# Performance work log

Hardware: AMD Instinct MI355X
Metric: run time of the kernel (lower is better)

The kernel has to match this reference:

```python
import jax, jax.numpy as jnp
import numpy as np

B, L, S, D, H = 32, 256, 64, 128, 4
DH = D // H
EPS = 1e-5


def _uniform(k, shape, scale):
    return jax.random.uniform(k, shape, jnp.float32, -scale, scale)


def setup_inputs() -> dict:
    key = jax.random.key(0)
    ks = jax.random.split(key, 12)
    sc = 1.0 / np.sqrt(D)
    return {
        "h_wq": jax.random.normal(ks[0], (B, L, D), jnp.float32),
        "h_all": jax.random.normal(ks[1], (B, L, S, D), jnp.float32),
        "station_id": jax.random.randint(ks[2], (B,), 0, S),
        "adj": jax.random.randint(ks[3], (S, S), 0, 2).astype(jnp.float32),
        "in_proj_w": _uniform(ks[4], (3 * D, D), sc),
        "in_proj_b": _uniform(ks[5], (3 * D,), sc),
        "out_w": _uniform(ks[6], (D, D), sc),
        "out_b": _uniform(ks[7], (D,), sc),
        "gate_w": _uniform(ks[8], (D, 2 * D), 1.0 / np.sqrt(2 * D)),
        "gate_b": _uniform(ks[9], (D,), 1.0 / np.sqrt(2 * D)),
        "ln_g": jnp.ones((D,), jnp.float32),
        "ln_b": jnp.zeros((D,), jnp.float32),
        "alpha": jnp.asarray(0.1, jnp.float32),
    }


def _allowed_mask(adj, station_id):
    # allowed[b, s] == True  <=> station s may attend as key for sample b
    sid = station_id.astype(jnp.int32)
    allowed = adj[sid] > 0.0                                  # [B, S]
    self_oh = jax.nn.one_hot(sid, adj.shape[0], dtype=bool)   # [B, S]
    allowed = allowed & ~self_oh                              # exclude self
    # fallback-to-all for rows with no neighbor (still excluding self)
    no_nb = ~jnp.any(allowed, axis=1, keepdims=True)
    allowed = jnp.where(no_nb, ~self_oh, allowed)
    # final safety: if STILL empty (S==1 edge case), allow self
    no_nb2 = ~jnp.any(allowed, axis=1, keepdims=True)
    allowed = allowed | (no_nb2 & self_oh)
    return allowed


def _forward(h_wq, h_all, station_id, adj, in_proj_w, in_proj_b,
             out_w, out_b, gate_w, gate_b, ln_g, ln_b, alpha):
    b, l, d = h_wq.shape
    s = h_all.shape[2]
    qw, kw, vw = jnp.split(in_proj_w, 3, axis=0)
    qb, kb, vb = jnp.split(in_proj_b, 3, axis=0)

    q = (h_wq @ qw.T + qb).reshape(b, l, H, DH)        # [B,L,H,DH]
    k = (h_all @ kw.T + kb).reshape(b, l, s, H, DH)    # [B,L,S,H,DH]
    v = (h_all @ vw.T + vb).reshape(b, l, s, H, DH)

    scores = jnp.einsum('blhd,blshd->blhs', q, k) / np.sqrt(DH)  # [B,L,H,S]
    allowed = _allowed_mask(adj, station_id)                     # [B,S]
    scores = jnp.where(allowed[:, None, None, :], scores, -jnp.inf)
    w = jax.nn.softmax(scores, axis=-1)

    ctx = jnp.einsum('blhs,blshd->blhd', w, v).reshape(b, l, d)
    ctx = ctx @ out_w.T + out_b                                  # out_proj

    g = jax.nn.sigmoid(jnp.concatenate([h_wq, ctx], axis=-1) @ gate_w.T + gate_b)
    y = h_wq + alpha * (g * ctx)                                 # dropout = eval mode

    mu = jnp.mean(y, axis=-1, keepdims=True)
    var = jnp.mean(jnp.square(y - mu), axis=-1, keepdims=True)
    return (y - mu) * jax.lax.rsqrt(var + EPS) * ln_g + ln_b


def reference(h_wq, h_all, station_id, adj, in_proj_w, in_proj_b,
              out_w, out_b, gate_w, gate_b, ln_g, ln_b, alpha):
    return _forward(h_wq, h_all, station_id, adj, in_proj_w, in_proj_b,
                    out_w, out_b, gate_w, gate_b, ln_g, ln_b, alpha)
```

## Files before the change

### kernel.cpp

```cpp
#include <hip/hip_runtime.h>
#include <math.h>

#define B_   32
#define L_   256
#define S_   64
#define D_   128
#define NTOK (B_*L_)
#define TPB  8

__global__ __launch_bounds__(256) void fused_kernel(
        const float* __restrict__ h_wq,  const float* __restrict__ h_all,
        const int* __restrict__ station_id, const float* __restrict__ adj,
        const float* __restrict__ in_proj_w, const float* __restrict__ in_proj_b,
        const float* __restrict__ out_w,  const float* __restrict__ out_b,
        const float* __restrict__ gate_w, const float* __restrict__ gate_b,
        const float* __restrict__ ln_g,   const float* __restrict__ ln_b,
        const float* __restrict__ alpha,  float* __restrict__ out) {
    __shared__ float X[TPB*132];
    __shared__ float QK[TPB*528];
    __shared__ float A[TPB*528];
    __shared__ float cb[TPB][4];
    __shared__ int   lst[64];
    __shared__ int   cnt_s;

    const int t0  = blockIdx.x * TPB;
    const int b   = t0 >> 8;
    const int tid = threadIdx.x;
    const int wv  = tid >> 6, lane = tid & 63;
    const int d   = tid & 127, pr = tid >> 7;
    const int tb  = 4*pr;
    const float scale = 0.17677669529663687f;

    if (tid < 64) {
        int sid = station_id[b];
        int s = tid;
        bool av = (adj[sid*S_ + s] > 0.0f) && (s != sid);
        unsigned long long m = __ballot(av);
        if (m == 0ull) { av = (s != sid); m = __ballot(av); }
        if (m == 0ull) { av = (s == sid); m = __ballot(av); }
        int idx = __popcll(m & ((1ull << s) - 1ull));
        if (av) lst[idx] = s;
        if (s == 0) cnt_s = __popcll(m);
    }
    {
        int tok = tid >> 5, d4 = tid & 31;
        *(float4*)&X[tok*132 + d4*4] =
            *(const float4*)(h_wq + (size_t)(t0 + tok)*128 + d4*4);
    }
    __syncthreads();

    {
        const float4* wrow = (const float4*)(in_proj_w + (size_t)d*128);
        const float qb = in_proj_b[d];
        float a0 = qb, a1 = qb, a2 = qb, a3 = qb;
        const float *x0 = &X[(tb+0)*132], *x1 = &X[(tb+1)*132];
        const float *x2 = &X[(tb+2)*132], *x3 = &X[(tb+3)*132];
        #pragma unroll 8
        for (int j4 = 0; j4 < 32; ++j4) {
            float4 w  = wrow[j4];
            float4 u0 = *(const float4*)(x0 + j4*4);
            float4 u1 = *(const float4*)(x1 + j4*4);
            float4 u2 = *(const float4*)(x2 + j4*4);
            float4 u3 = *(const float4*)(x3 + j4*4);
            a0 += w.x*u0.x + w.y*u0.y + w.z*u0.z + w.w*u0.w;
            a1 += w.x*u1.x + w.y*u1.y + w.z*u1.z + w.w*u1.w;
            a2 += w.x*u2.x + w.y*u2.y + w.z*u2.z + w.w*u2.w;
            a3 += w.x*u3.x + w.y*u3.y + w.z*u3.z + w.w*u3.w;
        }
        A[(tb+0)*132 + d] = a0;  A[(tb+1)*132 + d] = a1;
        A[(tb+2)*132 + d] = a2;  A[(tb+3)*132 + d] = a3;
    }
    __syncthreads();

    {
        #pragma unroll
        for (int h = 0; h < 4; ++h) {
            float a0 = 0.f, a1 = 0.f, a2 = 0.f, a3 = 0.f;
            const float* wcol = in_proj_w + (size_t)(128 + h*32)*128 + d;
            #pragma unroll 8
            for (int j = 0; j < 32; ++j) {
                float w = wcol[(size_t)j*128];
                a0 += w * A[(tb+0)*132 + h*32 + j];
                a1 += w * A[(tb+1)*132 + h*32 + j];
                a2 += w * A[(tb+2)*132 + h*32 + j];
                a3 += w * A[(tb+3)*132 + h*32 + j];
            }
            QK[(tb+0)*528 + h*132 + d] = a0 * scale;
            QK[(tb+1)*528 + h*132 + d] = a1 * scale;
            QK[(tb+2)*528 + h*132 + d] = a2 * scale;
            QK[(tb+3)*528 + h*132 + d] = a3 * scale;
        }
    }
    if (tid < 32) {
        int tok = tid >> 2, h = tid & 3;
        float s = 0.f;
        for (int j = 0; j < 32; ++j)
            s += A[tok*132 + h*32 + j] * in_proj_b[128 + h*32 + j];
        cb[tok][h] = s * scale;
    }
    __syncthreads();

    {
        const int cnt = cnt_s;
        #pragma unroll
        for (int k = 0; k < 2; ++k) {
            const int tl = 2*wv + k;
            const int ridx = lst[lane < cnt ? lane : 0];
            const float* base = h_all + (size_t)(t0 + tl)*(S_*D_);
            const float* rp = base + (size_t)ridx*D_;
            const float* qkb = &QK[tl*528];

            float s0 = cb[tl][0], s1 = cb[tl][1], s2 = cb[tl][2], s3 = cb[tl][3];
            #pragma unroll 8
            for (int j4 = 0; j4 < 32; ++j4) {
                float4 x  = *(const float4*)(rp + j4*4);
                float4 w0 = *(const float4*)(qkb + 0*132 + j4*4);
                float4 w1 = *(const float4*)(qkb + 1*132 + j4*4);
                float4 w2 = *(const float4*)(qkb + 2*132 + j4*4);
                float4 w3 = *(const float4*)(qkb + 3*132 + j4*4);
                s0 += w0.x*x.x + w0.y*x.y + w0.z*x.z + w0.w*x.w;
                s1 += w1.x*x.x + w1.y*x.y + w1.z*x.z + w1.w*x.w;
                s2 += w2.x*x.x + w2.y*x.y + w2.z*x.z + w2.w*x.w;
                s3 += w3.x*x.x + w3.y*x.y + w3.z*x.z + w3.w*x.w;
            }
            const bool act = (lane < cnt);
            if (!act) { s0 = s1 = s2 = s3 = -INFINITY; }

            float m0 = s0, m1 = s1, m2 = s2, m3 = s3;
            #pragma unroll
            for (int o = 32; o >= 1; o >>= 1) {
                m0 = fmaxf(m0, __shfl_xor(m0, o));
                m1 = fmaxf(m1, __shfl_xor(m1, o));
                m2 = fmaxf(m2, __shfl_xor(m2, o));
                m3 = fmaxf(m3, __shfl_xor(m3, o));
            }
            float p0 = act ? __expf(s0 - m0) : 0.f;
            float p1 = act ? __expf(s1 - m1) : 0.f;
            float p2 = act ? __expf(s2 - m2) : 0.f;
            float p3 = act ? __expf(s3 - m3) : 0.f;
            float q0 = p0, q1 = p1, q2 = p2, q3 = p3;
            #pragma unroll
            for (int o = 32; o >= 1; o >>= 1) {
                q0 += __shfl_xor(q0, o);
                q1 += __shfl_xor(q1, o);
                q2 += __shfl_xor(q2, o);
                q3 += __shfl_xor(q3, o);
            }
            float4 wv4;
            wv4.x = p0 / q0; wv4.y = p1 / q1; wv4.z = p2 / q2; wv4.w = p3 / q3;
            *(float4*)&QK[tl*528 + lane*4] = wv4;

            float2 u0 = {0,0}, u1 = {0,0}, u2 = {0,0}, u3 = {0,0};
            for (int i = 0; i < cnt; ++i) {
                float2 x = *(const float2*)(base + (size_t)lst[i]*D_ + 2*lane);
                float4 w = *(const float4*)&QK[tl*528 + i*4];
                u0.x += w.x*x.x; u0.y += w.x*x.y;
                u1.x += w.y*x.x; u1.y += w.y*x.y;
                u2.x += w.z*x.x; u2.y += w.z*x.y;
                u3.x += w.w*x.x; u3.y += w.w*x.y;
            }
            *(float2*)&A[tl*528 + 0*132 + 2*lane] = u0;
            *(float2*)&A[tl*528 + 1*132 + 2*lane] = u1;
            *(float2*)&A[tl*528 + 2*132 + 2*lane] = u2;
            *(float2*)&A[tl*528 + 3*132 + 2*lane] = u3;
        }
    }
    __syncthreads();

    {
        const int h = d >> 5;
        const float4* vwrow = (const float4*)(in_proj_w + (size_t)(256 + d)*128);
        const float vb = in_proj_b[256 + d];
        float a0 = vb, a1 = vb, a2 = vb, a3 = vb;
        const float *u0 = &A[(tb+0)*528 + h*132], *u1 = &A[(tb+1)*528 + h*132];
        const float *u2 = &A[(tb+2)*528 + h*132], *u3 = &A[(tb+3)*528 + h*132];
        #pragma unroll 8
        for (int j4 = 0; j4 < 32; ++j4) {
            float4 w  = vwrow[j4];
            float4 v0 = *(const float4*)(u0 + j4*4);
            float4 v1 = *(const float4*)(u1 + j4*4);
            float4 v2 = *(const float4*)(u2 + j4*4);
            float4 v3 = *(const float4*)(u3 + j4*4);
            a0 += w.x*v0.x + w.y*v0.y + w.z*v0.z + w.w*v0.w;
            a1 += w.x*v1.x + w.y*v1.y + w.z*v1.z + w.w*v1.w;
            a2 += w.x*v2.x + w.y*v2.y + w.z*v2.z + w.w*v2.w;
            a3 += w.x*v3.x + w.y*v3.y + w.z*v3.z + w.w*v3.w;
        }
        QK[(tb+0)*132 + d] = a0;  QK[(tb+1)*132 + d] = a1;
        QK[(tb+2)*132 + d] = a2;  QK[(tb+3)*132 + d] = a3;
    }
    __syncthreads();

    {
        const float4* wrow = (const float4*)(out_w + (size_t)d*128);
        const float ob = out_b[d];
        float a0 = ob, a1 = ob, a2 = ob, a3 = ob;
        const float *c0 = &QK[(tb+0)*132], *c1 = &QK[(tb+1)*132];
        const float *c2 = &QK[(tb+2)*132], *c3 = &QK[(tb+3)*132];
        #pragma unroll 8
        for (int j4 = 0; j4 < 32; ++j4) {
            float4 w  = wrow[j4];
            float4 v0 = *(const float4*)(c0 + j4*4);
            float4 v1 = *(const float4*)(c1 + j4*4);
            float4 v2 = *(const float4*)(c2 + j4*4);
            float4 v3 = *(const float4*)(c3 + j4*4);
            a0 += w.x*v0.x + w.y*v0.y + w.z*v0.z + w.w*v0.w;
            a1 += w.x*v1.x + w.y*v1.y + w.z*v1.z + w.w*v1.w;
            a2 += w.x*v2.x + w.y*v2.y + w.z*v2.z + w.w*v2.w;
            a3 += w.x*v3.x + w.y*v3.y + w.z*v3.z + w.w*v3.w;
        }
        __syncthreads();
        A[(tb+0)*132 + d] = a0;  A[(tb+1)*132 + d] = a1;
        A[(tb+2)*132 + d] = a2;  A[(tb+3)*132 + d] = a3;
    }
    __syncthreads();

    {
        const float4* wrow = (const float4*)(gate_w + (size_t)d*256);
        const float gb = gate_b[d];
        float g0 = gb, g1 = gb, g2 = gb, g3 = gb;
        const float *x0 = &X[(tb+0)*132], *x1 = &X[(tb+1)*132];
        const float *x2 = &X[(tb+2)*132], *x3 = &X[(tb+3)*132];
        const float *o0 = &A[(tb+0)*132], *o1 = &A[(tb+1)*132];
        const float *o2 = &A[(tb+2)*132], *o3 = &A[(tb+3)*132];
        #pragma unroll 4
        for (int j4 = 0; j4 < 32; ++j4) {
            float4 wx = wrow[j4];
            float4 wo = wrow[32 + j4];
            float4 a, o;
            a = *(const float4*)(x0 + j4*4); o = *(const float4*)(o0 + j4*4);
            g0 += wx.x*a.x + wx.y*a.y + wx.z*a.z + wx.w*a.w
                + wo.x*o.x + wo.y*o.y + wo.z*o.z + wo.w*o.w;
            a = *(const float4*)(x1 + j4*4); o = *(const float4*)(o1 + j4*4);
            g1 += wx.x*a.x + wx.y*a.y + wx.z*a.z + wx.w*a.w
                + wo.x*o.x + wo.y*o.y + wo.z*o.z + wo.w*o.w;
            a = *(const float4*)(x2 + j4*4); o = *(const float4*)(o2 + j4*4);
            g2 += wx.x*a.x + wx.y*a.y + wx.z*a.z + wx.w*a.w
                + wo.x*o.x + wo.y*o.y + wo.z*o.z + wo.w*o.w;
            a = *(const float4*)(x3 + j4*4); o = *(const float4*)(o3 + j4*4);
            g3 += wx.x*a.x + wx.y*a.y + wx.z*a.z + wx.w*a.w
                + wo.x*o.x + wo.y*o.y + wo.z*o.z + wo.w*o.w;
        }
        const float al = alpha[0];
        float s0 = 1.0f/(1.0f + __expf(-g0)), s1 = 1.0f/(1.0f + __expf(-g1));
        float s2 = 1.0f/(1.0f + __expf(-g2)), s3 = 1.0f/(1.0f + __expf(-g3));
        QK[1056 + (tb+0)*132 + d] = x0[d] + al*s0*o0[d];
        QK[1056 + (tb+1)*132 + d] = x1[d] + al*s1*o1[d];
        QK[1056 + (tb+2)*132 + d] = x2[d] + al*s2*o2[d];
        QK[1056 + (tb+3)*132 + d] = x3[d] + al*s3*o3[d];
    }
    __syncthreads();

    {
        #pragma unroll
        for (int k = 0; k < 2; ++k) {
            const int tl = 2*wv + k;
            float y0 = QK[1056 + tl*132 + lane];
            float y1 = QK[1056 + tl*132 + 64 + lane];
            float s = y0 + y1;
            #pragma unroll
            for (int o = 32; o >= 1; o >>= 1) s += __shfl_xor(s, o);
            float mu = s * (1.0f/128.0f);
            float d0 = y0 - mu, d1 = y1 - mu;
            float v = d0*d0 + d1*d1;
            #pragma unroll
            for (int o = 32; o >= 1; o >>= 1) v += __shfl_xor(v, o);
            float rs = rsqrtf(v*(1.0f/128.0f) + 1e-5f);
            out[(size_t)(t0 + tl)*128 + lane]      = d0*rs*ln_g[lane]    + ln_b[lane];
            out[(size_t)(t0 + tl)*128 + 64 + lane] = d1*rs*ln_g[64+lane] + ln_b[64+lane];
        }
    }
}

extern "C" void kernel_launch(void* const* d_in, const int* in_sizes, int n_in,
                              void* d_out, int out_size, void* d_ws, size_t ws_size,
                              hipStream_t stream) {
    const float* h_wq       = (const float*)d_in[0];
    const float* h_all      = (const float*)d_in[1];
    const int*   station_id = (const int*)  d_in[2];
    const float* adj        = (const float*)d_in[3];
    const float* in_proj_w  = (const float*)d_in[4];
    const float* in_proj_b  = (const float*)d_in[5];
    const float* out_w      = (const float*)d_in[6];
    const float* out_b      = (const float*)d_in[7];
    const float* gate_w     = (const float*)d_in[8];
    const float* gate_b     = (const float*)d_in[9];
    const float* ln_g       = (const float*)d_in[10];
    const float* ln_b       = (const float*)d_in[11];
    const float* alpha      = (const float*)d_in[12];
    float* out = (float*)d_out;

    fused_kernel<<<NTOK/TPB, 256, 0, stream>>>(
        h_wq, h_all, station_id, adj, in_proj_w, in_proj_b,
        out_w, out_b, gate_w, gate_b, ln_g, ln_b, alpha, out);
}
```

Baseline: 440.4 us.

## Compute attention scores with coalesced row loads and 16-lane shuffle reductions

Restructures the score computation so each 16-lane group handles one head and the wave loops over active neighbor rows, loading each h_all row contiguously instead of having each lane stream its own row. Partial dot products are reduced with width-16 xor shuffles and written to shared memory, then reloaded per lane for the softmax. This targets the uncoalesced per-lane row reads of h_all. In exchange it adds a serial loop over neighbors with shuffle reductions and an extra __syncthreads to protect the QK buffer reuse.

New measurement: 457.6 us. +3.9%, slower.

```diff
diff --git a/kernel.cpp b/kernel.cpp
--- a/kernel.cpp
+++ b/kernel.cpp
@@ -102,31 +102,32 @@
 
     {
         const int cnt = cnt_s;
+        const int g  = lane >> 4, lg = lane & 15;
         #pragma unroll
         for (int k = 0; k < 2; ++k) {
             const int tl = 2*wv + k;
-            const int ridx = lst[lane < cnt ? lane : 0];
             const float* base = h_all + (size_t)(t0 + tl)*(S_*D_);
-            const float* rp = base + (size_t)ridx*D_;
-            const float* qkb = &QK[tl*528];
-
-            float s0 = cb[tl][0], s1 = cb[tl][1], s2 = cb[tl][2], s3 = cb[tl][3];
-            #pragma unroll 8
-            for (int j4 = 0; j4 < 32; ++j4) {
-                float4 x  = *(const float4*)(rp + j4*4);
-                float4 w0 = *(const float4*)(qkb + 0*132 + j4*4);
-                float4 w1 = *(const float4*)(qkb + 1*132 + j4*4);
-                float4 w2 = *(const float4*)(qkb + 2*132 + j4*4);
-                float4 w3 = *(const float4*)(qkb + 3*132 + j4*4);
-                s0 += w0.x*x.x + w0.y*x.y + w0.z*x.z + w0.w*x.w;
-                s1 += w1.x*x.x + w1.y*x.y + w1.z*x.z + w1.w*x.w;
-                s2 += w2.x*x.x + w2.y*x.y + w2.z*x.z + w2.w*x.w;
-                s3 += w3.x*x.x + w3.y*x.y + w3.z*x.z + w3.w*x.w;
-            }
-            const bool act = (lane < cnt);
-            if (!act) { s0 = s1 = s2 = s3 = -INFINITY; }
-
-            float m0 = s0, m1 = s1, m2 = s2, m3 = s3;
+            const float4 qa  = *(const float4*)&QK[tl*528 + g*132 + 4*lg];
+            const float4 qb2 = *(const float4*)&QK[tl*528 + g*132 + 64 + 4*lg];
+            const float cbg = cb[tl][g];
+
+            for (int i = 0; i < cnt; ++i) {
+                const float* rp = base + (size_t)lst[i]*D_;
+                float4 xa = *(const float4*)(rp + 4*lg);
+                float4 xb = *(const float4*)(rp + 64 + 4*lg);
+                float p = qa.x*xa.x + qa.y*xa.y + qa.z*xa.z + qa.w*xa.w
+                        + qb2.x*xb.x + qb2.y*xb.y + qb2.z*xb.z + qb2.w*xb.w;
+                p += __shfl_xor(p, 8, 16);
+                p += __shfl_xor(p, 4, 16);
+                p += __shfl_xor(p, 2, 16);
+                p += __shfl_xor(p, 1, 16);
+                if (lg == 0) A[tl*528 + i*4 + g] = p + cbg;
+            }
+
+            float4 s4;
+            if (lane < cnt) s4 = *(const float4*)&A[tl*528 + lane*4];
+            else { s4.x = -INFINITY; s4.y = -INFINITY; s4.z = -INFINITY; s4.w = -INFINITY; }
+            float m0 = s4.x, m1 = s4.y, m2 = s4.z, m3 = s4.w;
             #pragma unroll
             for (int o = 32; o >= 1; o >>= 1) {
                 m0 = fmaxf(m0, __shfl_xor(m0, o));
@@ -134,10 +135,11 @@
                 m2 = fmaxf(m2, __shfl_xor(m2, o));
                 m3 = fmaxf(m3, __shfl_xor(m3, o));
             }
-            float p0 = act ? __expf(s0 - m0) : 0.f;
-            float p1 = act ? __expf(s1 - m1) : 0.f;
-            float p2 = act ? __expf(s2 - m2) : 0.f;
-            float p3 = act ? __expf(s3 - m3) : 0.f;
+            const bool act = (lane < cnt);
+            float p0 = act ? __expf(s4.x - m0) : 0.f;
+            float p1 = act ? __expf(s4.y - m1) : 0.f;
+            float p2 = act ? __expf(s4.z - m2) : 0.f;
+            float p3 = act ? __expf(s4.w - m3) : 0.f;
             float q0 = p0, q1 = p1, q2 = p2, q3 = p3;
             #pragma unroll
             for (int o = 32; o >= 1; o >>= 1) {
@@ -186,6 +188,7 @@
             a2 += w.x*v2.x + w.y*v2.y + w.z*v2.z + w.w*v2.w;
             a3 += w.x*v3.x + w.y*v3.y + w.z*v3.z + w.w*v3.w;
         }
+        __syncthreads();
         QK[(tb+0)*132 + d] = a0;  QK[(tb+1)*132 + d] = a1;
         QK[(tb+2)*132 + d] = a2;  QK[(tb+3)*132 + d] = a3;
     }
```
